# Kernel tuning notes

Measured on AMD Instinct MI355X. Metric: run time of the kernel, lower is better.

Reference implementation:

```python
import jax, jax.numpy as jnp
import numpy as np

B, C, S, Q = 4, 3, 5, 5
E = 90 * 768          # encoding_size for encoding_method != 1
N1 = B * C * S        # 60 support rows
N2 = B * C * Q        # 60 query rows
H = 32                # width of every Dense layer


def setup_inputs() -> dict:
    key = jax.random.key(0)
    ks = jax.random.split(key, 20)
    p = lambda k, shape: jax.random.normal(k, shape, jnp.float32) * 0.1
    return {
        "support_distance": jax.random.normal(ks[0], (N1, E), jnp.float32),
        "support_label": jax.random.randint(ks[1], (B, 15), 0, C, jnp.int32),
        "query_distance": jax.random.normal(ks[2], (N2, E), jnp.float32),
        # fvc_bar / gvc_bar (shared between distance and label paths)
        "W_fvc_bar": p(ks[3], (1, H)),  "b_fvc_bar": p(ks[4], (H,)),
        "W_gvc_bar": p(ks[5], (H, H)), "b_gvc_bar": p(ks[6], (H,)),
        # fu / gu (input to fu is concat([repeat(32-dim), 1-dim]) -> 33)
        "W_fu": p(ks[7], (H + 1, H)),  "b_fu": p(ks[8], (H,)),
        "W_gu": p(ks[9], (H, H)),      "b_gu": p(ks[10], (H,)),
        # fvc / gvc
        "W_fvc": p(ks[11], (H + 1, H)), "b_fvc": p(ks[12], (H,)),
        "W_gvc": p(ks[13], (H, H)),     "b_gvc": p(ks[14], (H,)),
        # fz / gz
        "W_fz": p(ks[15], (H + 1, H)),  "b_fz": p(ks[16], (H,)),
        "W_gz": p(ks[17], (H, H)),      "b_gz": p(ks[18], (H,)),
    }


def reference(support_distance, support_label, query_distance,
              W_fvc_bar, b_fvc_bar, W_gvc_bar, b_gvc_bar,
              W_fu, b_fu, W_gu, b_gu,
              W_fvc, b_fvc, W_gvc, b_gvc,
              W_fz, b_fz, W_gz, b_gz):
    relu = jax.nn.relu
    d1 = support_distance[..., None]                                   # [N1,E,1]
    # v_bar: fvc_bar over each scalar of the distance, mean over rows, then gvc_bar
    v_bar = relu(jnp.mean(relu(d1 @ W_fvc_bar + b_fvc_bar), axis=0)
                 @ W_gvc_bar + b_gvc_bar)                               # [E,32]
    # c_bar: same stack applied to one-hot labels
    lab = jax.nn.one_hot(support_label.reshape(N1).astype(jnp.int32), C)[..., None]  # [N1,C,1]
    c_bar = relu(jnp.mean(relu(lab @ W_fvc_bar + b_fvc_bar), axis=0)
                 @ W_gvc_bar + b_gvc_bar)                               # [C,32]
    # fu on concat([repeat(v_bar), d1]): split the 33-row weight to avoid concat
    Wu_v, wu_d = W_fu[:H], W_fu[H:]                                     # [32,32],[1,32]
    alpha = jnp.mean(relu((v_bar @ Wu_v)[None] + d1 * wu_d[0] + b_fu), axis=1)  # [N1,32]
    beta = jnp.mean(relu((c_bar @ Wu_v)[None] + lab * wu_d[0] + b_fu), axis=1)  # [N1,32]
    u_n = relu((alpha + beta) @ W_gu + b_gu)                            # [N1,32]
    # fvc on concat([repeat(u_n over E), d1]), mean over rows, gvc
    Wv_u, wv_d = W_fvc[:H], W_fvc[H:]
    v = relu(jnp.mean(relu((u_n @ Wv_u)[:, None, :] + d1 * wv_d[0] + b_fvc),
                      axis=0) @ W_gvc + b_gvc)                          # [E,32]
    # query branch: fz on concat([repeat(v), d2]), mean over E, gz
    d2 = query_distance[..., None]                                      # [N2,E,1]
    Wz_v, wz_d = W_fz[:H], W_fz[H:]
    z = jnp.mean(relu((v @ Wz_v)[None] + d2 * wz_d[0] + b_fz), axis=1)  # [N2,32]
    new_distance = relu(z @ W_gz + b_gz)                                # [N2,32]
    return new_distance.reshape(B, C, Q, H)
```

## Files before the change

kernel.cpp:

```cpp
#include <hip/hip_runtime.h>

#define E_DIM 69120
#define N1 60
#define H 32
#define CC 3
#define TEB 64
#define NB2 (E_DIM / TEB)
#define SDS 68
#define SBA 34
#define SBB 33
#define SBT 68
#define PSZ (N1 * H)


__device__ __forceinline__ float relu_dot4(const float4 d, const float w, const float4 t) {
    return fmaxf(fmaf(d.x, w, t.x), 0.f) + fmaxf(fmaf(d.y, w, t.y), 0.f)
         + fmaxf(fmaf(d.z, w, t.z), 0.f) + fmaxf(fmaf(d.w, w, t.w), 0.f);
}

template<bool ATOMIC>
__global__ __launch_bounds__(512, 4) void kA11(
    const float* __restrict__ d,
    const float* __restrict__ Wfvb, const float* __restrict__ bfvb,
    const float* __restrict__ Wgvb, const float* __restrict__ bgvb,
    const float* __restrict__ Wfu,  const float* __restrict__ bfu,
    float* __restrict__ outp)
{
    __shared__ __align__(16) float ds[N1 * SDS];
    __shared__ __align__(16) float bufAT[2176];
    __shared__ __align__(16) float bufB[64 * SBB];
    const int tid = threadIdx.x;
    const long sE = (long)blockIdx.x * TEB;

    for (int i = tid; i < N1 * (TEB / 4); i += 512) {
        const int n = i >> 4, c = (i & 15) * 4;
        *(float4*)(ds + n * SDS + c) = *(const float4*)(d + (long)n * E_DIM + sE + c);
    }
    __syncthreads();

    const int eL = tid & 63, h0 = (tid >> 6) * 4;

    {
        float wf[4], bf[4], ta[4], tb[4];
        #pragma unroll
        for (int j = 0; j < 4; ++j) {
            wf[j] = Wfvb[h0 + j] * (1.f / N1);
            bf[j] = bfvb[h0 + j] * (1.f / N1);
            ta[j] = 0.f; tb[j] = 0.f;
        }
        const float* dp = ds + eL;
        #pragma unroll 6
        for (int n = 0; n < N1; n += 2) {
            const float dv0 = dp[n * SDS];
            const float dv1 = dp[(n + 1) * SDS];
            #pragma unroll
            for (int j = 0; j < 4; ++j) {
                ta[j] += fmaxf(fmaf(dv0, wf[j], bf[j]), 0.f);
                tb[j] += fmaxf(fmaf(dv1, wf[j], bf[j]), 0.f);
            }
        }
        #pragma unroll
        for (int j = 0; j < 4; ++j) bufAT[eL * SBA + h0 + j] = ta[j] + tb[j];
    }
    __syncthreads();

    {
        float acc[4];
        #pragma unroll
        for (int j = 0; j < 4; ++j) acc[j] = bgvb[h0 + j];
        #pragma unroll
        for (int k = 0; k < H; ++k) {
            const float t = bufAT[eL * SBA + k];
            #pragma unroll
            for (int j = 0; j < 4; ++j) acc[j] = fmaf(t, Wgvb[k * H + h0 + j], acc[j]);
        }
        #pragma unroll
        for (int j = 0; j < 4; ++j) bufB[eL * SBB + h0 + j] = fmaxf(acc[j], 0.f);
    }
    __syncthreads();

    {
        float acc[4];
        #pragma unroll
        for (int j = 0; j < 4; ++j) acc[j] = bfu[h0 + j];
        #pragma unroll
        for (int k = 0; k < H; ++k) {
            const float t = bufB[eL * SBB + k];
            #pragma unroll
            for (int j = 0; j < 4; ++j) acc[j] = fmaf(t, Wfu[k * H + h0 + j], acc[j]);
        }
        #pragma unroll
        for (int j = 0; j < 4; ++j) bufAT[(h0 + j) * SBT + eL] = acc[j];
    }
    __syncthreads();

    if (tid < N1 * 8) {
        const int n = tid >> 3, hb4 = (tid & 7) * 4;
        float wud[4], acc[4];
        #pragma unroll
        for (int j = 0; j < 4; ++j) { wud[j] = Wfu[H * H + hb4 + j]; acc[j] = 0.f; }
        const float* dsrow = ds + n * SDS;
        for (int e8 = 0; e8 < TEB; e8 += 8) {
            const float4 dA = *(const float4*)(dsrow + e8);
            const float4 dB = *(const float4*)(dsrow + e8 + 4);
            #pragma unroll
            for (int j = 0; j < 4; ++j) {
                const float4 wA = *(const float4*)(bufAT + (hb4 + j) * SBT + e8);
                const float4 wB = *(const float4*)(bufAT + (hb4 + j) * SBT + e8 + 4);
                acc[j] += relu_dot4(dA, wud[j], wA) + relu_dot4(dB, wud[j], wB);
            }
        }
        if (ATOMIC) {
            float* p = outp + n * H + hb4;
            #pragma unroll
            for (int j = 0; j < 4; ++j) atomicAdd(&p[j], acc[j]);
        } else {
            *(float4*)(outp + (long)blockIdx.x * PSZ + n * H + hb4) =
                make_float4(acc[0], acc[1], acc[2], acc[3]);
        }
    }
}

template<bool ATOMIC>
__global__ __launch_bounds__(512, 4) void kCf11(
    const float* __restrict__ d, const float* __restrict__ d2,
    const float* __restrict__ uwb,
    const float* __restrict__ Wfvc,
    const float* __restrict__ Wgvc, const float* __restrict__ bgvc,
    const float* __restrict__ Wfz,  const float* __restrict__ bfz,
    float* __restrict__ outp)
{
    __shared__ __align__(16) float ds[N1 * SDS];
    __shared__ __align__(16) float bufAT[2176];
    __shared__ __align__(16) float bufB[64 * SBB];
    float* u_l = bufB;
    const int tid = threadIdx.x;
    const long sE = (long)blockIdx.x * TEB;

    for (int i = tid; i < N1 * (TEB / 4); i += 512) {
        const int n = i >> 4, c = (i & 15) * 4;
        *(float4*)(ds + n * SDS + c) = *(const float4*)(d + (long)n * E_DIM + sE + c);
    }
    if (tid < PSZ / 4) {
        float4 u = ((const float4*)uwb)[tid];
        u.x *= (1.f / N1); u.y *= (1.f / N1); u.z *= (1.f / N1); u.w *= (1.f / N1);
        ((float4*)u_l)[tid] = u;
    }
    __syncthreads();

    const int eL = tid & 63, h0 = (tid >> 6) * 4;

    {
        float wvd[4], ma[4], mb[4];
        #pragma unroll
        for (int j = 0; j < 4; ++j) { wvd[j] = Wfvc[H * H + h0 + j] * (1.f / N1); ma[j] = 0.f; mb[j] = 0.f; }
        const float* dp = ds + eL;
        #pragma unroll 6
        for (int n = 0; n < N1; n += 2) {
            const float dv0 = dp[n * SDS];
            const float dv1 = dp[(n + 1) * SDS];
            const float4 u0 = *(const float4*)(u_l + n * H + h0);
            const float4 u1 = *(const float4*)(u_l + (n + 1) * H + h0);
            ma[0] += fmaxf(fmaf(dv0, wvd[0], u0.x), 0.f);
            ma[1] += fmaxf(fmaf(dv0, wvd[1], u0.y), 0.f);
            ma[2] += fmaxf(fmaf(dv0, wvd[2], u0.z), 0.f);
            ma[3] += fmaxf(fmaf(dv0, wvd[3], u0.w), 0.f);
            mb[0] += fmaxf(fmaf(dv1, wvd[0], u1.x), 0.f);
            mb[1] += fmaxf(fmaf(dv1, wvd[1], u1.y), 0.f);
            mb[2] += fmaxf(fmaf(dv1, wvd[2], u1.z), 0.f);
            mb[3] += fmaxf(fmaf(dv1, wvd[3], u1.w), 0.f);
        }
        #pragma unroll
        for (int j = 0; j < 4; ++j) bufAT[eL * SBA + h0 + j] = ma[j] + mb[j];
    }
    __syncthreads();

    {
        float acc[4];
        #pragma unroll
        for (int j = 0; j < 4; ++j) acc[j] = bgvc[h0 + j];
        #pragma unroll
        for (int k = 0; k < H; ++k) {
            const float t = bufAT[eL * SBA + k];
            #pragma unroll
            for (int j = 0; j < 4; ++j) acc[j] = fmaf(t, Wgvc[k * H + h0 + j], acc[j]);
        }
        #pragma unroll
        for (int j = 0; j < 4; ++j) bufB[eL * SBB + h0 + j] = fmaxf(acc[j], 0.f);
    }
    __syncthreads();

    {
        float acc[4];
        #pragma unroll
        for (int j = 0; j < 4; ++j) acc[j] = bfz[h0 + j];
        #pragma unroll
        for (int k = 0; k < H; ++k) {
            const float t = bufB[eL * SBB + k];
            #pragma unroll
            for (int j = 0; j < 4; ++j) acc[j] = fmaf(t, Wfz[k * H + h0 + j], acc[j]);
        }
        #pragma unroll
        for (int j = 0; j < 4; ++j) bufAT[(h0 + j) * SBT + eL] = acc[j];
    }
    __syncthreads();

    if (tid < N1 * 8) {
        const int n = tid >> 3, hb4 = (tid & 7) * 4;
        float wzd[4], acc[4];
        #pragma unroll
        for (int j = 0; j < 4; ++j) { wzd[j] = Wfz[H * H + hb4 + j]; acc[j] = 0.f; }
        const float* drow = d2 + (long)n * E_DIM + sE;
        for (int e8 = 0; e8 < TEB; e8 += 8) {
            const float4 dA = *(const float4*)(drow + e8);
            const float4 dB = *(const float4*)(drow + e8 + 4);
            #pragma unroll
            for (int j = 0; j < 4; ++j) {
                const float4 wA = *(const float4*)(bufAT + (hb4 + j) * SBT + e8);
                const float4 wB = *(const float4*)(bufAT + (hb4 + j) * SBT + e8 + 4);
                acc[j] += relu_dot4(dA, wzd[j], wA) + relu_dot4(dB, wzd[j], wB);
            }
        }
        if (ATOMIC) {
            float* p = outp + n * H + hb4;
            #pragma unroll
            for (int j = 0; j < 4; ++j) atomicAdd(&p[j], acc[j]);
        } else {
            *(float4*)(outp + (long)blockIdx.x * PSZ + n * H + hb4) =
                make_float4(acc[0], acc[1], acc[2], acc[3]);
        }
    }
}

__global__ __launch_bounds__(256) void kR(
    const float* __restrict__ part, float* __restrict__ out)
{
    __shared__ float red[16][17];
    const int tid = threadIdx.x;
    const int oLoc = tid & 15, c = tid >> 4;
    const int o = blockIdx.x * 16 + oLoc;
    const int b0 = c * 68;
    const int bN = (NB2 - b0 < 68) ? (NB2 - b0) : 68;
    const float* p = part + (long)b0 * PSZ + o;
    float s = 0.f;
    #pragma unroll 4
    for (int b = 0; b < bN; ++b) s += p[(long)b * PSZ];
    red[c][oLoc] = s;
    __syncthreads();
    if (tid < 16) {
        float t = 0.f;
        #pragma unroll
        for (int ci = 0; ci < 16; ++ci) t += red[ci][tid];
        out[blockIdx.x * 16 + tid] = t;
    }
}

__global__ __launch_bounds__(1024) void kB(
    const float* __restrict__ alphaAcc, const int* __restrict__ label,
    const float* __restrict__ Wfvb, const float* __restrict__ bfvb,
    const float* __restrict__ Wgvb, const float* __restrict__ bgvb,
    const float* __restrict__ Wfu,  const float* __restrict__ bfu,
    const float* __restrict__ Wgu,  const float* __restrict__ bgu,
    const float* __restrict__ Wfvc, const float* __restrict__ bfvc,
    float* __restrict__ uwb)
{
    __shared__ float up_l[N1 * H];
    __shared__ float un_l[N1 * H];
    __shared__ float cb_l[CC * H];
    __shared__ float cw_l[CC * H];
    __shared__ int   cnt[CC];
    const int tid = threadIdx.x;

    if (tid < CC) cnt[tid] = 0;
    __syncthreads();
    if (tid < N1) atomicAdd(&cnt[label[tid]], 1);
    __syncthreads();

    if (tid < CC * H) {
        const int c = tid / H, h = tid % H;
        const float nc = (float)cnt[c];
        float s = bgvb[h];
        #pragma unroll
        for (int k = 0; k < H; ++k) {
            const float t1c = (nc * fmaxf(Wfvb[k] + bfvb[k], 0.f) +
                               ((float)N1 - nc) * fmaxf(bfvb[k], 0.f)) * (1.f / N1);
            s = fmaf(t1c, Wgvb[k * H + h], s);
        }
        cb_l[tid] = fmaxf(s, 0.f);
    }
    __syncthreads();
    if (tid < CC * H) {
        const int c = tid / H, h = tid % H;
        float s = bfu[h];
        #pragma unroll
        for (int k = 0; k < H; ++k) s = fmaf(cb_l[c * H + k], Wfu[k * H + h], s);
        cw_l[tid] = s;
    }
    __syncthreads();
    for (int t = tid; t < N1 * H; t += 1024) {
        const int n = t >> 5, h = t & 31;
        const int ln = label[n];
        const float wud = Wfu[H * H + h];
        float s = 0.f;
        #pragma unroll
        for (int c = 0; c < CC; ++c)
            s += fmaxf(cw_l[c * H + h] + ((c == ln) ? wud : 0.f), 0.f);
        up_l[t] = alphaAcc[t] * (1.f / E_DIM) + s * (1.f / CC);
    }
    __syncthreads();
    for (int t = tid; t < N1 * H; t += 1024) {
        const int n = t >> 5, h = t & 31;
        float s = bgu[h];
        #pragma unroll
        for (int k = 0; k < H; ++k) s = fmaf(up_l[n * H + k], Wgu[k * H + h], s);
        un_l[t] = fmaxf(s, 0.f);
    }
    __syncthreads();
    for (int t = tid; t < N1 * H; t += 1024) {
        const int n = t >> 5, h = t & 31;
        float s = bfvc[h];
        #pragma unroll
        for (int k = 0; k < H; ++k) s = fmaf(un_l[n * H + k], Wfvc[k * H + h], s);
        uwb[t] = s;
    }
}

__global__ __launch_bounds__(1024) void kD(
    const float* __restrict__ zAcc,
    const float* __restrict__ Wgz, const float* __restrict__ bgz,
    float* __restrict__ out)
{
    __shared__ float z_l[N1 * H];
    const int tid = threadIdx.x;
    for (int t = tid; t < N1 * H; t += 1024) z_l[t] = zAcc[t] * (1.f / E_DIM);
    __syncthreads();
    for (int t = tid; t < N1 * H; t += 1024) {
        const int n = t >> 5, h = t & 31;
        float s = bgz[h];
        #pragma unroll
        for (int k = 0; k < H; ++k) s = fmaf(z_l[n * H + k], Wgz[k * H + h], s);
        out[t] = fmaxf(s, 0.f);
    }
}

extern "C" void kernel_launch(void* const* d_in, const int* in_sizes, int n_in,
                              void* d_out, int out_size, void* d_ws, size_t ws_size,
                              hipStream_t stream)
{
    const float* sup  = (const float*)d_in[0];
    const int*   lab  = (const int*)d_in[1];
    const float* qry  = (const float*)d_in[2];
    const float* Wfvb = (const float*)d_in[3];
    const float* bfvb = (const float*)d_in[4];
    const float* Wgvb = (const float*)d_in[5];
    const float* bgvb = (const float*)d_in[6];
    const float* Wfu  = (const float*)d_in[7];
    const float* bfu  = (const float*)d_in[8];
    const float* Wgu  = (const float*)d_in[9];
    const float* bgu  = (const float*)d_in[10];
    const float* Wfvc = (const float*)d_in[11];
    const float* bfvc = (const float*)d_in[12];
    const float* Wgvc = (const float*)d_in[13];
    const float* bgvc = (const float*)d_in[14];
    const float* Wfz  = (const float*)d_in[15];
    const float* bfz  = (const float*)d_in[16];
    const float* Wgz  = (const float*)d_in[17];
    const float* bgz  = (const float*)d_in[18];
    float* out = (float*)d_out;

    float* alphaAcc = (float*)d_ws;
    float* zAcc     = alphaAcc + PSZ;
    float* uwb      = zAcc + PSZ;
    float* partA    = uwb + PSZ;
    float* partZ    = partA + (size_t)NB2 * PSZ;

    const size_t needMain = (3 * (size_t)PSZ + 2 * (size_t)NB2 * PSZ) * sizeof(float);

    if (ws_size >= needMain) {
        kA11<false><<<NB2, 512, 0, stream>>>(sup, Wfvb, bfvb, Wgvb, bgvb, Wfu, bfu, partA);
        kR<<<PSZ / 16, 256, 0, stream>>>(partA, alphaAcc);
        kB<<<1, 1024, 0, stream>>>(alphaAcc, lab, Wfvb, bfvb, Wgvb, bgvb, Wfu, bfu,
                                   Wgu, bgu, Wfvc, bfvc, uwb);
        kCf11<false><<<NB2, 512, 0, stream>>>(sup, qry, uwb, Wfvc, Wgvc, bgvc, Wfz, bfz, partZ);
        kR<<<PSZ / 16, 256, 0, stream>>>(partZ, zAcc);
        kD<<<1, 1024, 0, stream>>>(zAcc, Wgz, bgz, out);
    } else {
        (void)hipMemsetAsync(alphaAcc, 0, 2 * PSZ * sizeof(float), stream);
        kA11<true><<<NB2, 512, 0, stream>>>(sup, Wfvb, bfvb, Wgvb, bgvb, Wfu, bfu, alphaAcc);
        kB<<<1, 1024, 0, stream>>>(alphaAcc, lab, Wfvb, bfvb, Wgvb, bgvb, Wfu, bfu,
                                   Wgu, bgu, Wfvc, bfvc, uwb);
        kCf11<true><<<NB2, 512, 0, stream>>>(sup, qry, uwb, Wfvc, Wgvc, bgvc, Wfz, bfz, zAcc);
        kD<<<1, 1024, 0, stream>>>(zAcc, Wgz, bgz, out);
    }
}
```

Before: 103.9 us.

## Double E-tile per block, widen per-thread work, stage query tile in LDS

Raises the E tile per block from 64 to 128 columns, halving the block count and the size of the per-block partial sums that the reduction kernel reads. Each thread now computes 8 hidden outputs instead of 4, and rows are cached in registers before the small dense layers. In the final stage each thread handles two rows so the transposed weights it reads from LDS are reused, and that buffer uses a swizzled row index. The second kernel now copies the query tile into LDS instead of reading it from global memory in the last loop, and reads u directly from global memory. The trade-off is higher register and LDS use per block plus an extra sync, which may lower occupancy.

```diff
diff --git a/kernel.cpp b/kernel.cpp
--- a/kernel.cpp
+++ b/kernel.cpp
@@ -4,13 +4,13 @@
 #define N1 60
 #define H 32
 #define CC 3
-#define TEB 64
+#define TEB 128
 #define NB2 (E_DIM / TEB)
-#define SDS 68
-#define SBA 34
-#define SBB 33
-#define SBT 68
+#define SDS 132
+#define SBF 36
+#define TSTR 132
 #define PSZ (N1 * H)
+#define TROW(h) ((((h) & 3) << 3) | ((h) >> 2))
 
 
 __device__ __forceinline__ float relu_dot4(const float4 d, const float w, const float4 t) {
@@ -19,7 +19,7 @@
 }
 
 template<bool ATOMIC>
-__global__ __launch_bounds__(512, 4) void kA11(
+__global__ __launch_bounds__(512, 6) void kA13(
     const float* __restrict__ d,
     const float* __restrict__ Wfvb, const float* __restrict__ bfvb,
     const float* __restrict__ Wgvb, const float* __restrict__ bgvb,
@@ -27,102 +27,120 @@
     float* __restrict__ outp)
 {
     __shared__ __align__(16) float ds[N1 * SDS];
-    __shared__ __align__(16) float bufAT[2176];
-    __shared__ __align__(16) float bufB[64 * SBB];
+    __shared__ __align__(16) float buf[4608];
     const int tid = threadIdx.x;
     const long sE = (long)blockIdx.x * TEB;
 
     for (int i = tid; i < N1 * (TEB / 4); i += 512) {
-        const int n = i >> 4, c = (i & 15) * 4;
+        const int n = i >> 5, c = (i & 31) * 4;
         *(float4*)(ds + n * SDS + c) = *(const float4*)(d + (long)n * E_DIM + sE + c);
     }
     __syncthreads();
 
-    const int eL = tid & 63, h0 = (tid >> 6) * 4;
-
-    {
-        float wf[4], bf[4], ta[4], tb[4];
-        #pragma unroll
-        for (int j = 0; j < 4; ++j) {
-            wf[j] = Wfvb[h0 + j] * (1.f / N1);
-            bf[j] = bfvb[h0 + j] * (1.f / N1);
-            ta[j] = 0.f; tb[j] = 0.f;
-        }
+    const int eL = tid & 127, h0 = (tid >> 7) * 8;
+
+    {
+        float wf[8], bf[8], ta[8], tb[8];
+        #pragma unroll
+        for (int j = 0; j < 8; ++j) { wf[j] = Wfvb[h0+j]; bf[j] = bfvb[h0+j]; ta[j] = 0.f; tb[j] = 0.f; }
         const float* dp = ds + eL;
-        #pragma unroll 6
+        #pragma unroll 2
         for (int n = 0; n < N1; n += 2) {
             const float dv0 = dp[n * SDS];
             const float dv1 = dp[(n + 1) * SDS];
             #pragma unroll
-            for (int j = 0; j < 4; ++j) {
+            for (int j = 0; j < 8; ++j) {
                 ta[j] += fmaxf(fmaf(dv0, wf[j], bf[j]), 0.f);
                 tb[j] += fmaxf(fmaf(dv1, wf[j], bf[j]), 0.f);
             }
         }
-        #pragma unroll
-        for (int j = 0; j < 4; ++j) bufAT[eL * SBA + h0 + j] = ta[j] + tb[j];
-    }
-    __syncthreads();
-
-    {
-        float acc[4];
-        #pragma unroll
-        for (int j = 0; j < 4; ++j) acc[j] = bgvb[h0 + j];
+        float o[8];
+        #pragma unroll
+        for (int j = 0; j < 8; ++j) o[j] = (ta[j] + tb[j]) * (1.f / N1);
+        *(float4*)(buf + eL * SBF + h0)     = make_float4(o[0], o[1], o[2], o[3]);
+        *(float4*)(buf + eL * SBF + h0 + 4) = make_float4(o[4], o[5], o[6], o[7]);
+    }
+    __syncthreads();
+
+    float row[32];
+
+    #pragma unroll
+    for (int q = 0; q < 8; ++q)
+        *(float4*)(row + q * 4) = *(const float4*)(buf + eL * SBF + q * 4);
+    __syncthreads();
+    {
+        float acc[8];
+        #pragma unroll
+        for (int j = 0; j < 8; ++j) acc[j] = bgvb[h0 + j];
         #pragma unroll
         for (int k = 0; k < H; ++k) {
-            const float t = bufAT[eL * SBA + k];
-            #pragma unroll
-            for (int j = 0; j < 4; ++j) acc[j] = fmaf(t, Wgvb[k * H + h0 + j], acc[j]);
-        }
-        #pragma unroll
-        for (int j = 0; j < 4; ++j) bufB[eL * SBB + h0 + j] = fmaxf(acc[j], 0.f);
-    }
-    __syncthreads();
-
-    {
-        float acc[4];
-        #pragma unroll
-        for (int j = 0; j < 4; ++j) acc[j] = bfu[h0 + j];
+            const float t = row[k];
+            #pragma unroll
+            for (int j = 0; j < 8; ++j) acc[j] = fmaf(t, Wgvb[k * H + h0 + j], acc[j]);
+        }
+        #pragma unroll
+        for (int j = 0; j < 8; ++j) acc[j] = fmaxf(acc[j], 0.f);
+        *(float4*)(buf + eL * SBF + h0)     = make_float4(acc[0], acc[1], acc[2], acc[3]);
+        *(float4*)(buf + eL * SBF + h0 + 4) = make_float4(acc[4], acc[5], acc[6], acc[7]);
+    }
+    __syncthreads();
+
+    #pragma unroll
+    for (int q = 0; q < 8; ++q)
+        *(float4*)(row + q * 4) = *(const float4*)(buf + eL * SBF + q * 4);
+    __syncthreads();
+    {
+        float acc[8];
+        #pragma unroll
+        for (int j = 0; j < 8; ++j) acc[j] = bfu[h0 + j];
         #pragma unroll
         for (int k = 0; k < H; ++k) {
-            const float t = bufB[eL * SBB + k];
-            #pragma unroll
-            for (int j = 0; j < 4; ++j) acc[j] = fmaf(t, Wfu[k * H + h0 + j], acc[j]);
-        }
-        #pragma unroll
-        for (int j = 0; j < 4; ++j) bufAT[(h0 + j) * SBT + eL] = acc[j];
-    }
-    __syncthreads();
-
-    if (tid < N1 * 8) {
-        const int n = tid >> 3, hb4 = (tid & 7) * 4;
-        float wud[4], acc[4];
-        #pragma unroll
-        for (int j = 0; j < 4; ++j) { wud[j] = Wfu[H * H + hb4 + j]; acc[j] = 0.f; }
-        const float* dsrow = ds + n * SDS;
+            const float t = row[k];
+            #pragma unroll
+            for (int j = 0; j < 8; ++j) acc[j] = fmaf(t, Wfu[k * H + h0 + j], acc[j]);
+        }
+        #pragma unroll
+        for (int j = 0; j < 8; ++j) buf[TROW(h0 + j) * TSTR + eL] = acc[j];
+    }
+    __syncthreads();
+
+    if (tid < (N1 / 2) * 8) {
+        const int np = tid >> 3, hg = tid & 7, hb = hg * 4;
+        const int n0 = 2 * np, n1 = n0 + 1;
+        float wud[4], a0[4], a1[4];
+        #pragma unroll
+        for (int j = 0; j < 4; ++j) { wud[j] = Wfu[H * H + hb + j]; a0[j] = 0.f; a1[j] = 0.f; }
+        const float* r0 = ds + n0 * SDS;
+        const float* r1 = ds + n1 * SDS;
         for (int e8 = 0; e8 < TEB; e8 += 8) {
-            const float4 dA = *(const float4*)(dsrow + e8);
-            const float4 dB = *(const float4*)(dsrow + e8 + 4);
+            const float4 d0a = *(const float4*)(r0 + e8);
+            const float4 d0b = *(const float4*)(r0 + e8 + 4);
+            const float4 d1a = *(const float4*)(r1 + e8);
+            const float4 d1b = *(const float4*)(r1 + e8 + 4);
             #pragma unroll
             for (int j = 0; j < 4; ++j) {
-                const float4 wA = *(const float4*)(bufAT + (hb4 + j) * SBT + e8);
-                const float4 wB = *(const float4*)(bufAT + (hb4 + j) * SBT + e8 + 4);
-                acc[j] += relu_dot4(dA, wud[j], wA) + relu_dot4(dB, wud[j], wB);
+                const float* wr = buf + (j * 8 + hg) * TSTR + e8;
+                const float4 wA = *(const float4*)(wr);
+                const float4 wB = *(const float4*)(wr + 4);
+                a0[j] += relu_dot4(d0a, wud[j], wA) + relu_dot4(d0b, wud[j], wB);
+                a1[j] += relu_dot4(d1a, wud[j], wA) + relu_dot4(d1b, wud[j], wB);
             }
         }
         if (ATOMIC) {
-            float* p = outp + n * H + hb4;
-            #pragma unroll
-            for (int j = 0; j < 4; ++j) atomicAdd(&p[j], acc[j]);
+            float* p0 = outp + n0 * H + hb;
+            float* p1 = outp + n1 * H + hb;
+            #pragma unroll
+            for (int j = 0; j < 4; ++j) { atomicAdd(&p0[j], a0[j]); atomicAdd(&p1[j], a1[j]); }
         } else {
-            *(float4*)(outp + (long)blockIdx.x * PSZ + n * H + hb4) =
-                make_float4(acc[0], acc[1], acc[2], acc[3]);
+            float* base = outp + (long)blockIdx.x * PSZ;
+            *(float4*)(base + n0 * H + hb) = make_float4(a0[0], a0[1], a0[2], a0[3]);
+            *(float4*)(base + n1 * H + hb) = make_float4(a1[0], a1[1], a1[2], a1[3]);
         }
     }
 }
 
 template<bool ATOMIC>
-__global__ __launch_bounds__(512, 4) void kCf11(
+__global__ __launch_bounds__(512, 6) void kCf13(
     const float* __restrict__ d, const float* __restrict__ d2,
     const float* __restrict__ uwb,
     const float* __restrict__ Wfvc,
@@ -131,103 +149,124 @@
     float* __restrict__ outp)
 {
     __shared__ __align__(16) float ds[N1 * SDS];
-    __shared__ __align__(16) float bufAT[2176];
-    __shared__ __align__(16) float bufB[64 * SBB];
-    float* u_l = bufB;
+    __shared__ __align__(16) float buf[4608];
     const int tid = threadIdx.x;
     const long sE = (long)blockIdx.x * TEB;
 
     for (int i = tid; i < N1 * (TEB / 4); i += 512) {
-        const int n = i >> 4, c = (i & 15) * 4;
+        const int n = i >> 5, c = (i & 31) * 4;
         *(float4*)(ds + n * SDS + c) = *(const float4*)(d + (long)n * E_DIM + sE + c);
     }
-    if (tid < PSZ / 4) {
-        float4 u = ((const float4*)uwb)[tid];
-        u.x *= (1.f / N1); u.y *= (1.f / N1); u.z *= (1.f / N1); u.w *= (1.f / N1);
-        ((float4*)u_l)[tid] = u;
-    }
-    __syncthreads();
-
-    const int eL = tid & 63, h0 = (tid >> 6) * 4;
-
-    {
-        float wvd[4], ma[4], mb[4];
-        #pragma unroll
-        for (int j = 0; j < 4; ++j) { wvd[j] = Wfvc[H * H + h0 + j] * (1.f / N1); ma[j] = 0.f; mb[j] = 0.f; }
+    __syncthreads();
+
+    const int eL = tid & 127, h0 = (tid >> 7) * 8;
+
+    {
+        float wvd[8], ma[8], mb[8];
+        #pragma unroll
+        for (int j = 0; j < 8; ++j) { wvd[j] = Wfvc[H * H + h0 + j]; ma[j] = 0.f; mb[j] = 0.f; }
         const float* dp = ds + eL;
-        #pragma unroll 6
+        #pragma unroll 2
         for (int n = 0; n < N1; n += 2) {
             const float dv0 = dp[n * SDS];
             const float dv1 = dp[(n + 1) * SDS];
-            const float4 u0 = *(const float4*)(u_l + n * H + h0);
-            const float4 u1 = *(const float4*)(u_l + (n + 1) * H + h0);
-            ma[0] += fmaxf(fmaf(dv0, wvd[0], u0.x), 0.f);
-            ma[1] += fmaxf(fmaf(dv0, wvd[1], u0.y), 0.f);
-            ma[2] += fmaxf(fmaf(dv0, wvd[2], u0.z), 0.f);
-            ma[3] += fmaxf(fmaf(dv0, wvd[3], u0.w), 0.f);
-            mb[0] += fmaxf(fmaf(dv1, wvd[0], u1.x), 0.f);
-            mb[1] += fmaxf(fmaf(dv1, wvd[1], u1.y), 0.f);
-            mb[2] += fmaxf(fmaf(dv1, wvd[2], u1.z), 0.f);
-            mb[3] += fmaxf(fmaf(dv1, wvd[3], u1.w), 0.f);
-        }
-        #pragma unroll
-        for (int j = 0; j < 4; ++j) bufAT[eL * SBA + h0 + j] = ma[j] + mb[j];
-    }
-    __syncthreads();
-
-    {
-        float acc[4];
-        #pragma unroll
-        for (int j = 0; j < 4; ++j) acc[j] = bgvc[h0 + j];
+            const float4 u0a = *(const float4*)(uwb + n * H + h0);
+            const float4 u0b = *(const float4*)(uwb + n * H + h0 + 4);
+            const float4 u1a = *(const float4*)(uwb + (n + 1) * H + h0);
+            const float4 u1b = *(const float4*)(uwb + (n + 1) * H + h0 + 4);
+            const float u0[8] = {u0a.x,u0a.y,u0a.z,u0a.w,u0b.x,u0b.y,u0b.z,u0b.w};
+            const float u1[8] = {u1a.x,u1a.y,u1a.z,u1a.w,u1b.x,u1b.y,u1b.z,u1b.w};
+            #pragma unroll
+            for (int j = 0; j < 8; ++j) {
+                ma[j] += fmaxf(fmaf(dv0, wvd[j], u0[j]), 0.f);
+                mb[j] += fmaxf(fmaf(dv1, wvd[j], u1[j]), 0.f);
+            }
+        }
+        float o[8];
+        #pragma unroll
+        for (int j = 0; j < 8; ++j) o[j] = (ma[j] + mb[j]) * (1.f / N1);
+        *(float4*)(buf + eL * SBF + h0)     = make_float4(o[0], o[1], o[2], o[3]);
+        *(float4*)(buf + eL * SBF + h0 + 4) = make_float4(o[4], o[5], o[6], o[7]);
+    }
+    __syncthreads();
+
+    float row[32];
+
+    #pragma unroll
+    for (int q = 0; q < 8; ++q)
+        *(float4*)(row + q * 4) = *(const float4*)(buf + eL * SBF + q * 4);
+    for (int i = tid; i < N1 * (TEB / 4); i += 512) {
+        const int n = i >> 5, c = (i & 31) * 4;
+        *(float4*)(ds + n * SDS + c) = *(const float4*)(d2 + (long)n * E_DIM + sE + c);
+    }
+    __syncthreads();
+    {
+        float acc[8];
+        #pragma unroll
+        for (int j = 0; j < 8; ++j) acc[j] = bgvc[h0 + j];
         #pragma unroll
         for (int k = 0; k < H; ++k) {
-            const float t = bufAT[eL * SBA + k];
-            #pragma unroll
-            for (int j = 0; j < 4; ++j) acc[j] = fmaf(t, Wgvc[k * H + h0 + j], acc[j]);
-        }
-        #pragma unroll
-        for (int j = 0; j < 4; ++j) bufB[eL * SBB + h0 + j] = fmaxf(acc[j], 0.f);
-    }
-    __syncthreads();
-
-    {
-        float acc[4];
-        #pragma unroll
-        for (int j = 0; j < 4; ++j) acc[j] = bfz[h0 + j];
+            const float t = row[k];
+            #pragma unroll
+            for (int j = 0; j < 8; ++j) acc[j] = fmaf(t, Wgvc[k * H + h0 + j], acc[j]);
+        }
+        #pragma unroll
+        for (int j = 0; j < 8; ++j) acc[j] = fmaxf(acc[j], 0.f);
+        *(float4*)(buf + eL * SBF + h0)     = make_float4(acc[0], acc[1], acc[2], acc[3]);
+        *(float4*)(buf + eL * SBF + h0 + 4) = make_float4(acc[4], acc[5], acc[6], acc[7]);
+    }
+    __syncthreads();
+
+    #pragma unroll
+    for (int q = 0; q < 8; ++q)
+        *(float4*)(row + q * 4) = *(const float4*)(buf + eL * SBF + q * 4);
+    __syncthreads();
+    {
+        float acc[8];
+        #pragma unroll
+        for (int j = 0; j < 8; ++j) acc[j] = bfz[h0 + j];
         #pragma unroll
         for (int k = 0; k < H; ++k) {
-            const float t = bufB[eL * SBB + k];
-            #pragma unroll
-            for (int j = 0; j < 4; ++j) acc[j] = fmaf(t, Wfz[k * H + h0 + j], acc[j]);
-        }
-        #pragma unroll
-        for (int j = 0; j < 4; ++j) bufAT[(h0 + j) * SBT + eL] = acc[j];
-    }
-    __syncthreads();
-
-    if (tid < N1 * 8) {
-        const int n = tid >> 3, hb4 = (tid & 7) * 4;
-        float wzd[4], acc[4];
-        #pragma unroll
-        for (int j = 0; j < 4; ++j) { wzd[j] = Wfz[H * H + hb4 + j]; acc[j] = 0.f; }
-        const float* drow = d2 + (long)n * E_DIM + sE;
+            const float t = row[k];
+            #pragma unroll
+            for (int j = 0; j < 8; ++j) acc[j] = fmaf(t, Wfz[k * H + h0 + j], acc[j]);
+        }
+        #pragma unroll
+        for (int j = 0; j < 8; ++j) buf[TROW(h0 + j) * TSTR + eL] = acc[j];
+    }
+    __syncthreads();
+
+    if (tid < (N1 / 2) * 8) {
+        const int np = tid >> 3, hg = tid & 7, hb = hg * 4;
+        const int n0 = 2 * np, n1 = n0 + 1;
+        float wzd[4], a0[4], a1[4];
+        #pragma unroll
+        for (int j = 0; j < 4; ++j) { wzd[j] = Wfz[H * H + hb + j]; a0[j] = 0.f; a1[j] = 0.f; }
+        const float* r0 = ds + n0 * SDS;
+        const float* r1 = ds + n1 * SDS;
         for (int e8 = 0; e8 < TEB; e8 += 8) {
-            const float4 dA = *(const float4*)(drow + e8);
-            const float4 dB = *(const float4*)(drow + e8 + 4);
+            const float4 d0a = *(const float4*)(r0 + e8);
+            const float4 d0b = *(const float4*)(r0 + e8 + 4);
+            const float4 d1a = *(const float4*)(r1 + e8);
+            const float4 d1b = *(const float4*)(r1 + e8 + 4);
             #pragma unroll
             for (int j = 0; j < 4; ++j) {
-                const float4 wA = *(const float4*)(bufAT + (hb4 + j) * SBT + e8);
-                const float4 wB = *(const float4*)(bufAT + (hb4 + j) * SBT + e8 + 4);
-                acc[j] += relu_dot4(dA, wzd[j], wA) + relu_dot4(dB, wzd[j], wB);
+                const float* wr = buf + (j * 8 + hg) * TSTR + e8;
+                const float4 wA = *(const float4*)(wr);
+                const float4 wB = *(const float4*)(wr + 4);
+                a0[j] += relu_dot4(d0a, wzd[j], wA) + relu_dot4(d0b, wzd[j], wB);
+                a1[j] += relu_dot4(d1a, wzd[j], wA) + relu_dot4(d1b, wzd[j], wB);
             }
         }
         if (ATOMIC) {
-            float* p = outp + n * H + hb4;
-            #pragma unroll
-            for (int j = 0; j < 4; ++j) atomicAdd(&p[j], acc[j]);
+            float* p0 = outp + n0 * H + hb;
+            float* p1 = outp + n1 * H + hb;
+            #pragma unroll
+            for (int j = 0; j < 4; ++j) { atomicAdd(&p0[j], a0[j]); atomicAdd(&p1[j], a1[j]); }
         } else {
-            *(float4*)(outp + (long)blockIdx.x * PSZ + n * H + hb4) =
-                make_float4(acc[0], acc[1], acc[2], acc[3]);
+            float* base = outp + (long)blockIdx.x * PSZ;
+            *(float4*)(base + n0 * H + hb) = make_float4(a0[0], a0[1], a0[2], a0[3]);
+            *(float4*)(base + n1 * H + hb) = make_float4(a1[0], a1[1], a1[2], a1[3]);
         }
     }
 }
@@ -239,11 +278,11 @@
     const int tid = threadIdx.x;
     const int oLoc = tid & 15, c = tid >> 4;
     const int o = blockIdx.x * 16 + oLoc;
-    const int b0 = c * 68;
-    const int bN = (NB2 - b0 < 68) ? (NB2 - b0) : 68;
+    const int b0 = c * 34;
+    const int bN = (NB2 - b0 < 34) ? (NB2 - b0) : 34;
     const float* p = part + (long)b0 * PSZ + o;
     float s = 0.f;
-    #pragma unroll 4
+    #pragma unroll 2
     for (int b = 0; b < bN; ++b) s += p[(long)b * PSZ];
     red[c][oLoc] = s;
     __syncthreads();
@@ -377,19 +416,19 @@
     const size_t needMain = (3 * (size_t)PSZ + 2 * (size_t)NB2 * PSZ) * sizeof(float);
 
     if (ws_size >= needMain) {
-        kA11<false><<<NB2, 512, 0, stream>>>(sup, Wfvb, bfvb, Wgvb, bgvb, Wfu, bfu, partA);
+        kA13<false><<<NB2, 512, 0, stream>>>(sup, Wfvb, bfvb, Wgvb, bgvb, Wfu, bfu, partA);
         kR<<<PSZ / 16, 256, 0, stream>>>(partA, alphaAcc);
         kB<<<1, 1024, 0, stream>>>(alphaAcc, lab, Wfvb, bfvb, Wgvb, bgvb, Wfu, bfu,
                                    Wgu, bgu, Wfvc, bfvc, uwb);
-        kCf11<false><<<NB2, 512, 0, stream>>>(sup, qry, uwb, Wfvc, Wgvc, bgvc, Wfz, bfz, partZ);
+        kCf13<false><<<NB2, 512, 0, stream>>>(sup, qry, uwb, Wfvc, Wgvc, bgvc, Wfz, bfz, partZ);
         kR<<<PSZ / 16, 256, 0, stream>>>(partZ, zAcc);
         kD<<<1, 1024, 0, stream>>>(zAcc, Wgz, bgz, out);
     } else {
         (void)hipMemsetAsync(alphaAcc, 0, 2 * PSZ * sizeof(float), stream);
-        kA11<true><<<NB2, 512, 0, stream>>>(sup, Wfvb, bfvb, Wgvb, bgvb, Wfu, bfu, alphaAcc);
+        kA13<true><<<NB2, 512, 0, stream>>>(sup, Wfvb, bfvb, Wgvb, bgvb, Wfu, bfu, alphaAcc);
         kB<<<1, 1024, 0, stream>>>(alphaAcc, lab, Wfvb, bfvb, Wgvb, bgvb, Wfu, bfu,
                                    Wgu, bgu, Wfvc, bfvc, uwb);
-        kCf11<true><<<NB2, 512, 0, stream>>>(sup, qry, uwb, Wfvc, Wgvc, bgvc, Wfz, bfz, zAcc);
+        kCf13<true><<<NB2, 512, 0, stream>>>(sup, qry, uwb, Wfvc, Wgvc, bgvc, Wfz, bfz, zAcc);
         kD<<<1, 1024, 0, stream>>>(zAcc, Wgz, bgz, out);
     }
 }
```

New measurement: 134.4 us. 1.29x slower.
